# Performance work log

Hardware: AMD Instinct MI355X
Metric: run time of the kernel (lower is better)

Reference implementation:

```python
import jax, jax.numpy as jnp
import numpy as np

N_NODES = 100000


def _degrees(src, dst):
    ones = jnp.ones(src.shape[0], dtype=jnp.float32)
    out_deg = jax.ops.segment_sum(ones, src, num_segments=N_NODES)
    in_deg = jax.ops.segment_sum(ones, dst, num_segments=N_NODES)
    # DGL clamps degrees to a minimum of 1 before the power
    inv_sqrt_out = jax.lax.rsqrt(jnp.maximum(out_deg, 1.0))
    inv_sqrt_in = jax.lax.rsqrt(jnp.maximum(in_deg, 1.0))
    return inv_sqrt_out, inv_sqrt_in


def _graph_conv(h, W, b, src, dst, inv_sqrt_out, inv_sqrt_in):
    # DGL GraphConv, norm='both': D_out^{-1/2} on src feats, SpMM-sum, D_in^{-1/2} on dst
    h = h * inv_sqrt_out[:, None]
    h = h @ W  # applying weight before aggregation is mathematically identical
    agg = jax.ops.segment_sum(h[src], dst, num_segments=N_NODES)
    return agg * inv_sqrt_in[:, None] + b


def setup_inputs() -> dict:
    key = jax.random.key(0)
    ks = jax.random.split(key, 6)
    E, IN, HID = 1600000, 128, 128
    scale = 1.0 / np.sqrt(IN)
    return {
        "feat": jax.random.normal(ks[0], (N_NODES, IN), dtype=jnp.float32),
        "W0": jax.random.normal(ks[1], (IN, HID), dtype=jnp.float32) * scale,
        "b0": jnp.zeros((HID,), dtype=jnp.float32),
        "W1": jax.random.normal(ks[2], (HID, HID), dtype=jnp.float32) * scale,
        "b1": jnp.zeros((HID,), dtype=jnp.float32),
        "W2": jax.random.normal(ks[3], (HID, HID), dtype=jnp.float32) * scale,
        "b2": jnp.zeros((HID,), dtype=jnp.float32),
        "src": jax.random.randint(ks[4], (E,), 0, N_NODES, dtype=jnp.int32),
        "dst": jax.random.randint(ks[5], (E,), 0, N_NODES, dtype=jnp.int32),
    }


def reference(feat, W0, b0, W1, b1, W2, b2, src, dst):
    inv_sqrt_out, inv_sqrt_in = _degrees(src, dst)
    skips = [feat]
    h = feat
    for W, b in ((W0, b0), (W1, b1), (W2, b2)):
        h = jax.nn.relu(_graph_conv(h, W, b, src, dst, inv_sqrt_out, inv_sqrt_in))
        skips.append(h)
    return jnp.concatenate(skips, axis=1)  # torch.hstack on 2D == concat along dim 1
```

## Files before the change

kernel.cpp:

```cpp
#include <hip/hip_runtime.h>
#include <hip/hip_fp16.h>

#define NN 100000
#define NE 1600000
#define FD 128
#define OS 512
#define LDA 136
#define NBKT 196
#define PCH 4096

typedef __attribute__((ext_vector_type(8))) short short8;
typedef __attribute__((ext_vector_type(4))) float f32x4;

__device__ __forceinline__ short f2bf(float x) {
    unsigned u = __float_as_uint(x);
    u = (u + 0x7fff + ((u >> 16) & 1)) >> 16;
    return (short)u;
}

__global__ void k_init_out(const float* __restrict__ feat, float* __restrict__ out) {
    const size_t total = (size_t)NN * 32;
    for (size_t i = (size_t)blockIdx.x * blockDim.x + threadIdx.x; i < total;
         i += (size_t)gridDim.x * blockDim.x) {
        size_t n = i >> 5;
        int c4 = (int)(i & 31);
        ((float4*)(out + n * OS))[c4] = ((const float4*)feat)[n * 32 + c4];
    }
}

__global__ void k_prep_w(const float* __restrict__ W0, const float* __restrict__ W1,
                         const float* __restrict__ W2, short* __restrict__ Wt) {
    int i = blockIdx.x * blockDim.x + threadIdx.x;
    if (i >= 3 * FD * FD) return;
    int l = i >> 14, r = i & (FD * FD - 1);
    int n = r >> 7, k = r & 127;
    const float* W = (l == 0) ? W0 : ((l == 1) ? W1 : W2);
    Wt[i] = f2bf(W[k * FD + n]);
}

__global__ __launch_bounds__(256) void k_deg(const int* __restrict__ src,
                                             const int* __restrict__ dst,
                                             int* __restrict__ bktcnt_d,
                                             int* __restrict__ bktcnt_s) {
    __shared__ int hd[NBKT];
    __shared__ int hs[NBKT];
    for (int i = threadIdx.x; i < NBKT; i += 256) { hd[i] = 0; hs[i] = 0; }
    __syncthreads();
    const int total4 = NE / 4;
    for (int i = blockIdx.x * blockDim.x + threadIdx.x; i < total4;
         i += gridDim.x * blockDim.x) {
        int4 s = ((const int4*)src)[i];
        int4 d = ((const int4*)dst)[i];
        atomicAdd(&hs[s.x >> 9], 1); atomicAdd(&hs[s.y >> 9], 1);
        atomicAdd(&hs[s.z >> 9], 1); atomicAdd(&hs[s.w >> 9], 1);
        atomicAdd(&hd[d.x >> 9], 1); atomicAdd(&hd[d.y >> 9], 1);
        atomicAdd(&hd[d.z >> 9], 1); atomicAdd(&hd[d.w >> 9], 1);
    }
    __syncthreads();
    for (int i = threadIdx.x; i < NBKT; i += 256) {
        if (hd[i]) atomicAdd(&bktcnt_d[i], hd[i]);
        if (hs[i]) atomicAdd(&bktcnt_s[i], hs[i]);
    }
}

__global__ __launch_bounds__(256) void k_scan2(const int* __restrict__ bktcnt_d,
                                               const int* __restrict__ bktcnt_s,
                                               int* __restrict__ base_d,
                                               int* __restrict__ cur_d,
                                               int* __restrict__ base_s,
                                               int* __restrict__ cur_s) {
    __shared__ int sh[256];
    const int tid = threadIdx.x;
    int v = (tid < NBKT) ? bktcnt_d[tid] : 0;
    sh[tid] = v;
    __syncthreads();
    for (int off = 1; off < 256; off <<= 1) {
        int t = (tid >= off) ? sh[tid - off] : 0;
        __syncthreads();
        sh[tid] += t;
        __syncthreads();
    }
    int excl = sh[tid] - v;
    if (tid < NBKT) { base_d[tid] = excl; cur_d[tid] = excl; }
    if (tid == NBKT - 1) base_d[NBKT] = excl + v;
    __syncthreads();
    v = (tid < NBKT) ? bktcnt_s[tid] : 0;
    sh[tid] = v;
    __syncthreads();
    for (int off = 1; off < 256; off <<= 1) {
        int t = (tid >= off) ? sh[tid - off] : 0;
        __syncthreads();
        sh[tid] += t;
        __syncthreads();
    }
    excl = sh[tid] - v;
    if (tid < NBKT) { base_s[tid] = excl; cur_s[tid] = excl; }
    if (tid == NBKT - 1) base_s[NBKT] = excl + v;
}

__global__ __launch_bounds__(256) void k_part(const int* __restrict__ src,
                                              const int* __restrict__ dst,
                                              int* __restrict__ cur_d,
                                              int* __restrict__ cur_s,
                                              int2* __restrict__ pairs,
                                              unsigned short* __restrict__ ssrc) {
    __shared__ int hd[NBKT], bd[NBKT], ld_[NBKT];
    __shared__ int hs_[NBKT], bs_[NBKT], ls_[NBKT];
    const int tid = threadIdx.x;
    const int e0 = blockIdx.x * PCH;
    for (int i = tid; i < NBKT; i += 256) { hd[i] = 0; ld_[i] = 0; hs_[i] = 0; ls_[i] = 0; }
    __syncthreads();
    int md[16], ms[16];
    #pragma unroll
    for (int k = 0; k < 16; ++k) {
        int e = e0 + k * 256 + tid;
        md[k] = (e < NE) ? dst[e] : -1;
        ms[k] = (e < NE) ? src[e] : -1;
    }
    #pragma unroll
    for (int k = 0; k < 16; ++k)
        if (md[k] >= 0) {
            atomicAdd(&hd[md[k] >> 9], 1);
            atomicAdd(&hs_[ms[k] >> 9], 1);
        }
    __syncthreads();
    for (int i = tid; i < NBKT; i += 256) {
        bd[i] = hd[i] ? atomicAdd(&cur_d[i], hd[i]) : 0;
        bs_[i] = hs_[i] ? atomicAdd(&cur_s[i], hs_[i]) : 0;
    }
    __syncthreads();
    #pragma unroll
    for (int k = 0; k < 16; ++k)
        if (md[k] >= 0) {
            int b = md[k] >> 9;
            int off = atomicAdd(&ld_[b], 1);
            pairs[bd[b] + off] = make_int2(ms[k], md[k]);
            int b2 = ms[k] >> 9;
            int off2 = atomicAdd(&ls_[b2], 1);
            ssrc[bs_[b2] + off2] = (unsigned short)(ms[k] & 511);
        }
}

__global__ __launch_bounds__(256) void k_build(const int2* __restrict__ pairs,
                                               const int* __restrict__ bkt_base,
                                               int* __restrict__ row_ptr,
                                               int* __restrict__ col,
                                               float* __restrict__ inv_in) {
    __shared__ int cnt_s[512];
    __shared__ int wsum[4];
    const int b = blockIdx.x;
    const int tid = threadIdx.x;
    const int lane = tid & 63, wid = tid >> 6;
    const int ebeg = bkt_base[b], eend = bkt_base[b + 1];
    const int n0 = b << 9;
    cnt_s[tid] = 0; cnt_s[tid + 256] = 0;
    __syncthreads();
    for (int e = ebeg + tid; e < eend; e += 256)
        atomicAdd(&cnt_s[pairs[e].y - n0], 1);
    __syncthreads();
    const int v0 = cnt_s[2 * tid], v1 = cnt_s[2 * tid + 1];
    const int sum2 = v0 + v1;
    int incl = sum2;
    #pragma unroll
    for (int off = 1; off < 64; off <<= 1) {
        int t = __shfl_up(incl, off, 64);
        if (lane >= off) incl += t;
    }
    if (lane == 63) wsum[wid] = incl;
    __syncthreads();
    if (tid == 0) {
        int c = 0;
        #pragma unroll
        for (int i = 0; i < 4; ++i) { int t = wsum[i]; wsum[i] = c; c += t; }
    }
    __syncthreads();
    const int e0 = wsum[wid] + incl - sum2;
    cnt_s[2 * tid] = e0;
    cnt_s[2 * tid + 1] = e0 + v0;
    const int g0 = n0 + 2 * tid, g1 = g0 + 1;
    if (g0 < NN) { row_ptr[g0] = ebeg + e0; inv_in[g0] = rsqrtf((float)max(v0, 1)); }
    if (g1 < NN) { row_ptr[g1] = ebeg + e0 + v0; inv_in[g1] = rsqrtf((float)max(v1, 1)); }
    if (b == NBKT - 1 && tid == 0) row_ptr[NN] = eend;
    __syncthreads();
    for (int e = ebeg + tid; e < eend; e += 256) {
        int2 p = pairs[e];
        int pos = atomicAdd(&cnt_s[p.y - n0], 1);
        col[ebeg + pos] = p.x;
    }
}

__global__ __launch_bounds__(256) void k_build_src(const unsigned short* __restrict__ ssrc,
                                                   const int* __restrict__ base_s,
                                                   float* __restrict__ inv_out) {
    __shared__ int cnt_s[512];
    const int b = blockIdx.x;
    const int tid = threadIdx.x;
    const int ebeg = base_s[b], eend = base_s[b + 1];
    cnt_s[tid] = 0; cnt_s[tid + 256] = 0;
    __syncthreads();
    for (int e = ebeg + tid; e < eend; e += 256)
        atomicAdd(&cnt_s[ssrc[e]], 1);
    __syncthreads();
    const int n0 = b << 9;
    const int g0 = n0 + tid, g1 = g0 + 256;
    if (g0 < NN) inv_out[g0] = rsqrtf((float)max(cnt_s[tid], 1));
    if (g1 < NN) inv_out[g1] = rsqrtf((float)max(cnt_s[tid + 256], 1));
}

__global__ __launch_bounds__(256) void k_gemm(const float* __restrict__ h, int hstride,
                                              const short* __restrict__ Wt,
                                              const float* __restrict__ inv_out,
                                              unsigned char* __restrict__ tmp8,
                                              float* __restrict__ scales) {
    __shared__ short Ws[FD * LDA];
    __shared__ short hA[64 * LDA];
    const int tid = threadIdx.x;
    for (int i = tid; i < FD * 16; i += 256) {
        int n = i >> 4, c = i & 15;
        short8 v = *(const short8*)(Wt + n * FD + c * 8);
        *(short8*)(&Ws[n * LDA + c * 8]) = v;
    }
    const int row0 = blockIdx.x * 128;
    const int wid = tid >> 6, lane = tid & 63;
    const int m = lane & 15, quad = lane >> 4;

    for (int sub = 0; sub < 2; ++sub) {
        const int rbase = row0 + sub * 64;
        __syncthreads();
        for (int i = tid; i < 64 * 32; i += 256) {
            int r = i >> 5, c4 = i & 31;
            int gr = rbase + r;
            float4 v = make_float4(0.f, 0.f, 0.f, 0.f);
            if (gr < NN) v = ((const float4*)(h + (size_t)gr * hstride))[c4];
            short4 b;
            b.x = f2bf(v.x); b.y = f2bf(v.y); b.z = f2bf(v.z); b.w = f2bf(v.w);
            *(short4*)(&hA[r * LDA + c4 * 4]) = b;
        }
        __syncthreads();
        const int rtile = rbase + wid * 16;
        short8 a0 = *(const short8*)(&hA[(wid * 16 + m) * LDA + 0 * 32 + quad * 8]);
        short8 a1 = *(const short8*)(&hA[(wid * 16 + m) * LDA + 1 * 32 + quad * 8]);
        short8 a2 = *(const short8*)(&hA[(wid * 16 + m) * LDA + 2 * 32 + quad * 8]);
        short8 a3 = *(const short8*)(&hA[(wid * 16 + m) * LDA + 3 * 32 + quad * 8]);
        float s0, s1, s2, s3;
        {
            int r = rtile + quad * 4;
            s0 = (r + 0 < NN) ? inv_out[r + 0] : 0.f;
            s1 = (r + 1 < NN) ? inv_out[r + 1] : 0.f;
            s2 = (r + 2 < NN) ? inv_out[r + 2] : 0.f;
            s3 = (r + 3 < NN) ? inv_out[r + 3] : 0.f;
        }
        f32x4 accs[8];
        #pragma unroll
        for (int ct = 0; ct < 8; ++ct) {
            f32x4 acc = {0.f, 0.f, 0.f, 0.f};
            short8 b0 = *(const short8*)(&Ws[(ct * 16 + m) * LDA + 0 * 32 + quad * 8]);
            short8 b1 = *(const short8*)(&Ws[(ct * 16 + m) * LDA + 1 * 32 + quad * 8]);
            short8 b2 = *(const short8*)(&Ws[(ct * 16 + m) * LDA + 2 * 32 + quad * 8]);
            short8 b3 = *(const short8*)(&Ws[(ct * 16 + m) * LDA + 3 * 32 + quad * 8]);
            acc = __builtin_amdgcn_mfma_f32_16x16x32_bf16(a0, b0, acc, 0, 0, 0);
            acc = __builtin_amdgcn_mfma_f32_16x16x32_bf16(a1, b1, acc, 0, 0, 0);
            acc = __builtin_amdgcn_mfma_f32_16x16x32_bf16(a2, b2, acc, 0, 0, 0);
            acc = __builtin_amdgcn_mfma_f32_16x16x32_bf16(a3, b3, acc, 0, 0, 0);
            acc[0] *= s0; acc[1] *= s1; acc[2] *= s2; acc[3] *= s3;
            accs[ct] = acc;
        }
        float pm0 = 0.f, pm1 = 0.f, pm2 = 0.f, pm3 = 0.f;
        #pragma unroll
        for (int ct = 0; ct < 8; ++ct) {
            pm0 = fmaxf(pm0, fabsf(accs[ct][0]));
            pm1 = fmaxf(pm1, fabsf(accs[ct][1]));
            pm2 = fmaxf(pm2, fabsf(accs[ct][2]));
            pm3 = fmaxf(pm3, fabsf(accs[ct][3]));
        }
        #pragma unroll
        for (int off = 1; off < 16; off <<= 1) {
            pm0 = fmaxf(pm0, __shfl_xor(pm0, off));
            pm1 = fmaxf(pm1, __shfl_xor(pm1, off));
            pm2 = fmaxf(pm2, __shfl_xor(pm2, off));
            pm3 = fmaxf(pm3, __shfl_xor(pm3, off));
        }
        const float is0 = pm0 > 0.f ? 127.f / pm0 : 0.f;
        const float is1 = pm1 > 0.f ? 127.f / pm1 : 0.f;
        const float is2 = pm2 > 0.f ? 127.f / pm2 : 0.f;
        const float is3 = pm3 > 0.f ? 127.f / pm3 : 0.f;
        const int r = rtile + quad * 4;
        if (m == 0) {
            const float inv127 = 1.f / 127.f;
            if (r + 3 < NN) {
                float4 sv = make_float4(pm0 * inv127, pm1 * inv127, pm2 * inv127, pm3 * inv127);
                *((float4*)(scales + r)) = sv;
            } else {
                if (r + 0 < NN) scales[r + 0] = pm0 * inv127;
                if (r + 1 < NN) scales[r + 1] = pm1 * inv127;
                if (r + 2 < NN) scales[r + 2] = pm2 * inv127;
                if (r + 3 < NN) scales[r + 3] = pm3 * inv127;
            }
        }
        unsigned long long w0 = 0ull, w1 = 0ull, w2 = 0ull, w3 = 0ull;
        #pragma unroll
        for (int ct = 0; ct < 8; ++ct) {
            unsigned char q0 = (unsigned char)(char)(int)rintf(accs[ct][0] * is0);
            unsigned char q1 = (unsigned char)(char)(int)rintf(accs[ct][1] * is1);
            unsigned char q2 = (unsigned char)(char)(int)rintf(accs[ct][2] * is2);
            unsigned char q3 = (unsigned char)(char)(int)rintf(accs[ct][3] * is3);
            w0 |= (unsigned long long)q0 << (8 * ct);
            w1 |= (unsigned long long)q1 << (8 * ct);
            w2 |= (unsigned long long)q2 << (8 * ct);
            w3 |= (unsigned long long)q3 << (8 * ct);
        }
        unsigned char* base = tmp8 + (size_t)r * FD + m * 8;
        if (r + 3 < NN) {
            *(unsigned long long*)(base + 0 * FD) = w0;
            *(unsigned long long*)(base + 1 * FD) = w1;
            *(unsigned long long*)(base + 2 * FD) = w2;
            *(unsigned long long*)(base + 3 * FD) = w3;
        } else {
            if (r + 0 < NN) *(unsigned long long*)(base + 0 * FD) = w0;
            if (r + 1 < NN) *(unsigned long long*)(base + 1 * FD) = w1;
            if (r + 2 < NN) *(unsigned long long*)(base + 2 * FD) = w2;
            if (r + 3 < NN) *(unsigned long long*)(base + 3 * FD) = w3;
        }
    }
}

__global__ __launch_bounds__(256) void k_gather(const unsigned char* __restrict__ tmp8,
                                                const float* __restrict__ scales,
                                                const int* __restrict__ row_ptr,
                                                const int* __restrict__ col,
                                                const float* __restrict__ inv_in,
                                                const float* __restrict__ bias,
                                                float* __restrict__ out, int off) {
    __shared__ float ob_s[4][128];
    const int wid = threadIdx.x >> 6;
    const int lane = threadIdx.x & 63;
    const int half = lane >> 5;
    const int sl = lane & 31;
    const int node = blockIdx.x * 4 + wid;
    if (node >= NN) return;
    const int beg = row_ptr[node], end = row_ptr[node + 1];
    float a0 = 0.f, a1 = 0.f, a2 = 0.f, a3 = 0.f;
    int j = beg + half;
    for (; j + 6 < end; j += 8) {
        int s0 = col[j], s1 = col[j + 2], s2 = col[j + 4], s3 = col[j + 6];
        char4 c0 = *(const char4*)(tmp8 + (size_t)s0 * FD + sl * 4);
        char4 c1 = *(const char4*)(tmp8 + (size_t)s1 * FD + sl * 4);
        char4 c2 = *(const char4*)(tmp8 + (size_t)s2 * FD + sl * 4);
        char4 c3 = *(const char4*)(tmp8 + (size_t)s3 * FD + sl * 4);
        float f0 = scales[s0], f1 = scales[s1], f2 = scales[s2], f3 = scales[s3];
        a0 += f0 * (float)c0.x + f1 * (float)c1.x + f2 * (float)c2.x + f3 * (float)c3.x;
        a1 += f0 * (float)c0.y + f1 * (float)c1.y + f2 * (float)c2.y + f3 * (float)c3.y;
        a2 += f0 * (float)c0.z + f1 * (float)c1.z + f2 * (float)c2.z + f3 * (float)c3.z;
        a3 += f0 * (float)c0.w + f1 * (float)c1.w + f2 * (float)c2.w + f3 * (float)c3.w;
    }
    for (; j < end; j += 2) {
        int s0 = col[j];
        char4 c0 = *(const char4*)(tmp8 + (size_t)s0 * FD + sl * 4);
        float f0 = scales[s0];
        a0 += f0 * (float)c0.x;
        a1 += f0 * (float)c0.y;
        a2 += f0 * (float)c0.z;
        a3 += f0 * (float)c0.w;
    }
    a0 += __shfl_xor(a0, 32);
    a1 += __shfl_xor(a1, 32);
    a2 += __shfl_xor(a2, 32);
    a3 += __shfl_xor(a3, 32);
    if (half == 0) {
        float av[4] = {a0, a1, a2, a3};
        #pragma unroll
        for (int k = 0; k < 4; ++k) {
            int jj = 4 * sl + k;
            int c = ((jj & 7) << 4) + (jj >> 3);
            ob_s[wid][c] = av[k];
        }
        const float s = inv_in[node];
        float4 f4 = ((const float4*)ob_s[wid])[sl];
        const float4 bb = ((const float4*)bias)[sl];
        float4 r;
        r.x = fmaxf(f4.x * s + bb.x, 0.f);
        r.y = fmaxf(f4.y * s + bb.y, 0.f);
        r.z = fmaxf(f4.z * s + bb.z, 0.f);
        r.w = fmaxf(f4.w * s + bb.w, 0.f);
        ((float4*)(out + (size_t)node * OS + off))[sl] = r;
    }
}

extern "C" void kernel_launch(void* const* d_in, const int* in_sizes, int n_in,
                              void* d_out, int out_size, void* d_ws, size_t ws_size,
                              hipStream_t stream) {
    const float* feat = (const float*)d_in[0];
    const float* W0 = (const float*)d_in[1];
    const float* b0 = (const float*)d_in[2];
    const float* W1 = (const float*)d_in[3];
    const float* b1 = (const float*)d_in[4];
    const float* W2 = (const float*)d_in[5];
    const float* b2 = (const float*)d_in[6];
    const int* src = (const int*)d_in[7];
    const int* dst = (const int*)d_in[8];
    float* out = (float*)d_out;
    float* ws = (float*)d_ws;

    unsigned char* tmp8 = (unsigned char*)ws;
    int2* pairs = (int2*)(ws + (size_t)NN * 64);
    float* scales = ws + (size_t)NN * 96;
    unsigned short* ssrc = (unsigned short*)(ws + (size_t)NN * 104);
    int* base2 = (int*)(ws + (size_t)NN * 128);
    int* bktcnt_d = base2;
    int* bktcnt_s = bktcnt_d + NBKT;
    int* base_d = bktcnt_s + NBKT;
    int* cur_d = base_d + NBKT + 1;
    int* base_s = cur_d + NBKT;
    int* cur_s = base_s + NBKT + 1;
    float* inv = (float*)(cur_s + NBKT);
    int* row_ptr = (int*)(inv + 2 * NN);
    int* col = row_ptr + NN + 1;
    short* Wt = (short*)(col + NE);

    hipMemsetAsync(bktcnt_d, 0, 2 * NBKT * sizeof(int), stream);
    k_init_out<<<4096, 256, 0, stream>>>(feat, out);
    k_prep_w<<<(3 * FD * FD + 255) / 256, 256, 0, stream>>>(W0, W1, W2, Wt);
    k_deg<<<512, 256, 0, stream>>>(src, dst, bktcnt_d, bktcnt_s);
    k_scan2<<<1, 256, 0, stream>>>(bktcnt_d, bktcnt_s, base_d, cur_d, base_s, cur_s);
    k_part<<<(NE + PCH - 1) / PCH, 256, 0, stream>>>(src, dst, cur_d, cur_s, pairs, ssrc);
    k_build<<<NBKT, 256, 0, stream>>>(pairs, base_d, row_ptr, col, inv + NN);
    k_build_src<<<NBKT, 256, 0, stream>>>(ssrc, base_s, inv);

    const float* bs[3] = {b0, b1, b2};
    const float* h = feat;
    int hstride = FD;
    for (int l = 0; l < 3; ++l) {
        k_gemm<<<(NN + 127) / 128, 256, 0, stream>>>(h, hstride, Wt + l * FD * FD, inv,
                                                     tmp8, scales);
        k_gather<<<(NN + 3) / 4, 256, 0, stream>>>(tmp8, scales, row_ptr, col, inv + NN,
                                                   bs[l], out, FD * (l + 1));
        h = out + FD * (l + 1);
        hstride = OS;
    }
}
```

Measured before the change: 566.0 us.

## Keep bf16 copy of hidden features for GEMM input; merge build kernels; nontemporal I/O

The producer kernels (init_out and gather) now also write a bf16 copy of each layer's activations to a workspace buffer. The GEMM reads these bf16 rows directly instead of fp32 rows from the strided output and converting them. This roughly halves GEMM input traffic at the cost of an extra small write per layer. The src-degree build is merged into k_build as extra blocks to save a launch, and nontemporal loads/stores are used for col indices and output writes to reduce cache pollution.

Measured after the change: 583.0 us. +3.0%, slower.

```diff
diff --git a/kernel.cpp b/kernel.cpp
--- a/kernel.cpp
+++ b/kernel.cpp
@@ -18,13 +18,18 @@
     return (short)u;
 }
 
-__global__ void k_init_out(const float* __restrict__ feat, float* __restrict__ out) {
+__global__ void k_init_out(const float* __restrict__ feat, float* __restrict__ out,
+                           short* __restrict__ hb) {
     const size_t total = (size_t)NN * 32;
     for (size_t i = (size_t)blockIdx.x * blockDim.x + threadIdx.x; i < total;
          i += (size_t)gridDim.x * blockDim.x) {
         size_t n = i >> 5;
         int c4 = (int)(i & 31);
-        ((float4*)(out + n * OS))[c4] = ((const float4*)feat)[n * 32 + c4];
+        f32x4 v = ((const f32x4*)feat)[n * 32 + c4];
+        __builtin_nontemporal_store(v, ((f32x4*)(out + n * OS)) + c4);
+        short4 b;
+        b.x = f2bf(v.x); b.y = f2bf(v.y); b.z = f2bf(v.z); b.w = f2bf(v.w);
+        *(short4*)(hb + n * FD + c4 * 4) = b;
     }
 }
 
@@ -142,16 +147,33 @@
 }
 
 __global__ __launch_bounds__(256) void k_build(const int2* __restrict__ pairs,
-                                               const int* __restrict__ bkt_base,
+                                               const int* __restrict__ base_d,
+                                               const unsigned short* __restrict__ ssrc,
+                                               const int* __restrict__ base_s,
                                                int* __restrict__ row_ptr,
                                                int* __restrict__ col,
-                                               float* __restrict__ inv_in) {
+                                               float* __restrict__ inv_in,
+                                               float* __restrict__ inv_out) {
     __shared__ int cnt_s[512];
     __shared__ int wsum[4];
+    const int tid = threadIdx.x;
+    if (blockIdx.x >= NBKT) {
+        const int b = blockIdx.x - NBKT;
+        const int ebeg = base_s[b], eend = base_s[b + 1];
+        cnt_s[tid] = 0; cnt_s[tid + 256] = 0;
+        __syncthreads();
+        for (int e = ebeg + tid; e < eend; e += 256)
+            atomicAdd(&cnt_s[ssrc[e]], 1);
+        __syncthreads();
+        const int n0 = b << 9;
+        const int g0 = n0 + tid, g1 = g0 + 256;
+        if (g0 < NN) inv_out[g0] = rsqrtf((float)max(cnt_s[tid], 1));
+        if (g1 < NN) inv_out[g1] = rsqrtf((float)max(cnt_s[tid + 256], 1));
+        return;
+    }
     const int b = blockIdx.x;
-    const int tid = threadIdx.x;
     const int lane = tid & 63, wid = tid >> 6;
-    const int ebeg = bkt_base[b], eend = bkt_base[b + 1];
+    const int ebeg = base_d[b], eend = base_d[b + 1];
     const int n0 = b << 9;
     cnt_s[tid] = 0; cnt_s[tid + 256] = 0;
     __syncthreads();
@@ -189,25 +211,7 @@
     }
 }
 
-__global__ __launch_bounds__(256) void k_build_src(const unsigned short* __restrict__ ssrc,
-                                                   const int* __restrict__ base_s,
-                                                   float* __restrict__ inv_out) {
-    __shared__ int cnt_s[512];
-    const int b = blockIdx.x;
-    const int tid = threadIdx.x;
-    const int ebeg = base_s[b], eend = base_s[b + 1];
-    cnt_s[tid] = 0; cnt_s[tid + 256] = 0;
-    __syncthreads();
-    for (int e = ebeg + tid; e < eend; e += 256)
-        atomicAdd(&cnt_s[ssrc[e]], 1);
-    __syncthreads();
-    const int n0 = b << 9;
-    const int g0 = n0 + tid, g1 = g0 + 256;
-    if (g0 < NN) inv_out[g0] = rsqrtf((float)max(cnt_s[tid], 1));
-    if (g1 < NN) inv_out[g1] = rsqrtf((float)max(cnt_s[tid + 256], 1));
-}
-
-__global__ __launch_bounds__(256) void k_gemm(const float* __restrict__ h, int hstride,
+__global__ __launch_bounds__(256) void k_gemm(const short* __restrict__ hb,
                                               const short* __restrict__ Wt,
                                               const float* __restrict__ inv_out,
                                               unsigned char* __restrict__ tmp8,
@@ -227,14 +231,12 @@
     for (int sub = 0; sub < 2; ++sub) {
         const int rbase = row0 + sub * 64;
         __syncthreads();
-        for (int i = tid; i < 64 * 32; i += 256) {
-            int r = i >> 5, c4 = i & 31;
+        for (int i = tid; i < 64 * 16; i += 256) {
+            int r = i >> 4, c = i & 15;
             int gr = rbase + r;
-            float4 v = make_float4(0.f, 0.f, 0.f, 0.f);
-            if (gr < NN) v = ((const float4*)(h + (size_t)gr * hstride))[c4];
-            short4 b;
-            b.x = f2bf(v.x); b.y = f2bf(v.y); b.z = f2bf(v.z); b.w = f2bf(v.w);
-            *(short4*)(&hA[r * LDA + c4 * 4]) = b;
+            short8 v = {0, 0, 0, 0, 0, 0, 0, 0};
+            if (gr < NN) v = *(const short8*)(hb + (size_t)gr * FD + c * 8);
+            *(short8*)(&hA[r * LDA + c * 8]) = v;
         }
         __syncthreads();
         const int rtile = rbase + wid * 16;
@@ -288,8 +290,8 @@
         if (m == 0) {
             const float inv127 = 1.f / 127.f;
             if (r + 3 < NN) {
-                float4 sv = make_float4(pm0 * inv127, pm1 * inv127, pm2 * inv127, pm3 * inv127);
-                *((float4*)(scales + r)) = sv;
+                f32x4 sv = {pm0 * inv127, pm1 * inv127, pm2 * inv127, pm3 * inv127};
+                *((f32x4*)(scales + r)) = sv;
             } else {
                 if (r + 0 < NN) scales[r + 0] = pm0 * inv127;
                 if (r + 1 < NN) scales[r + 1] = pm1 * inv127;
@@ -330,7 +332,8 @@
                                                 const int* __restrict__ col,
                                                 const float* __restrict__ inv_in,
                                                 const float* __restrict__ bias,
-                                                float* __restrict__ out, int off) {
+                                                float* __restrict__ out, int off,
+                                                short* __restrict__ hb) {
     __shared__ float ob_s[4][128];
     const int wid = threadIdx.x >> 6;
     const int lane = threadIdx.x & 63;
@@ -342,7 +345,10 @@
     float a0 = 0.f, a1 = 0.f, a2 = 0.f, a3 = 0.f;
     int j = beg + half;
     for (; j + 6 < end; j += 8) {
-        int s0 = col[j], s1 = col[j + 2], s2 = col[j + 4], s3 = col[j + 6];
+        int s0 = __builtin_nontemporal_load(col + j);
+        int s1 = __builtin_nontemporal_load(col + j + 2);
+        int s2 = __builtin_nontemporal_load(col + j + 4);
+        int s3 = __builtin_nontemporal_load(col + j + 6);
         char4 c0 = *(const char4*)(tmp8 + (size_t)s0 * FD + sl * 4);
         char4 c1 = *(const char4*)(tmp8 + (size_t)s1 * FD + sl * 4);
         char4 c2 = *(const char4*)(tmp8 + (size_t)s2 * FD + sl * 4);
@@ -354,7 +360,7 @@
         a3 += f0 * (float)c0.w + f1 * (float)c1.w + f2 * (float)c2.w + f3 * (float)c3.w;
     }
     for (; j < end; j += 2) {
-        int s0 = col[j];
+        int s0 = __builtin_nontemporal_load(col + j);
         char4 c0 = *(const char4*)(tmp8 + (size_t)s0 * FD + sl * 4);
         float f0 = scales[s0];
         a0 += f0 * (float)c0.x;
@@ -375,14 +381,19 @@
             ob_s[wid][c] = av[k];
         }
         const float s = inv_in[node];
-        float4 f4 = ((const float4*)ob_s[wid])[sl];
-        const float4 bb = ((const float4*)bias)[sl];
-        float4 r;
+        f32x4 f4 = ((const f32x4*)ob_s[wid])[sl];
+        const f32x4 bb = ((const f32x4*)bias)[sl];
+        f32x4 r;
         r.x = fmaxf(f4.x * s + bb.x, 0.f);
         r.y = fmaxf(f4.y * s + bb.y, 0.f);
         r.z = fmaxf(f4.z * s + bb.z, 0.f);
         r.w = fmaxf(f4.w * s + bb.w, 0.f);
-        ((float4*)(out + (size_t)node * OS + off))[sl] = r;
+        __builtin_nontemporal_store(r, ((f32x4*)(out + (size_t)node * OS + off)) + sl);
+        if (hb) {
+            short4 hq;
+            hq.x = f2bf(r.x); hq.y = f2bf(r.y); hq.z = f2bf(r.z); hq.w = f2bf(r.w);
+            *(short4*)(hb + (size_t)node * FD + sl * 4) = hq;
+        }
     }
 }
 
@@ -402,10 +413,11 @@
     float* ws = (float*)d_ws;
 
     unsigned char* tmp8 = (unsigned char*)ws;
-    int2* pairs = (int2*)(ws + (size_t)NN * 64);
-    float* scales = ws + (size_t)NN * 96;
-    unsigned short* ssrc = (unsigned short*)(ws + (size_t)NN * 104);
-    int* base2 = (int*)(ws + (size_t)NN * 128);
+    short* hb = (short*)(ws + (size_t)NN * 32);
+    int2* pairs = (int2*)(ws + (size_t)NN * 96);
+    unsigned short* ssrc = (unsigned short*)(ws + (size_t)NN * 128);
+    float* scales = ws + (size_t)NN * 136;
+    int* base2 = (int*)(ws + (size_t)NN * 137);
     int* bktcnt_d = base2;
     int* bktcnt_s = bktcnt_d + NBKT;
     int* base_d = bktcnt_s + NBKT;
@@ -418,23 +430,20 @@
     short* Wt = (short*)(col + NE);
 
     hipMemsetAsync(bktcnt_d, 0, 2 * NBKT * sizeof(int), stream);
-    k_init_out<<<4096, 256, 0, stream>>>(feat, out);
+    k_init_out<<<4096, 256, 0, stream>>>(feat, out, hb);
     k_prep_w<<<(3 * FD * FD + 255) / 256, 256, 0, stream>>>(W0, W1, W2, Wt);
     k_deg<<<512, 256, 0, stream>>>(src, dst, bktcnt_d, bktcnt_s);
     k_scan2<<<1, 256, 0, stream>>>(bktcnt_d, bktcnt_s, base_d, cur_d, base_s, cur_s);
     k_part<<<(NE + PCH - 1) / PCH, 256, 0, stream>>>(src, dst, cur_d, cur_s, pairs, ssrc);
-    k_build<<<NBKT, 256, 0, stream>>>(pairs, base_d, row_ptr, col, inv + NN);
-    k_build_src<<<NBKT, 256, 0, stream>>>(ssrc, base_s, inv);
+    k_build<<<2 * NBKT, 256, 0, stream>>>(pairs, base_d, ssrc, base_s, row_ptr, col,
+                                          inv + NN, inv);
 
     const float* bs[3] = {b0, b1, b2};
-    const float* h = feat;
-    int hstride = FD;
     for (int l = 0; l < 3; ++l) {
-        k_gemm<<<(NN + 127) / 128, 256, 0, stream>>>(h, hstride, Wt + l * FD * FD, inv,
+        k_gemm<<<(NN + 127) / 128, 256, 0, stream>>>(hb, Wt + l * FD * FD, inv,
                                                      tmp8, scales);
         k_gather<<<(NN + 3) / 4, 256, 0, stream>>>(tmp8, scales, row_ptr, col, inv + NN,
-                                                   bs[l], out, FD * (l + 1));
-        h = out + FD * (l + 1);
-        hstride = OS;
-    }
-}
+                                                   bs[l], out, FD * (l + 1),
+                                                   (l < 2) ? hb : (short*)nullptr);
+    }
+}
```
